# Performance work log

Hardware: AMD Instinct MI355X
Metric: run time of the kernel (lower is better)

The kernel has to match this reference:

```python
import jax, jax.numpy as jnp
import numpy as np
from jax import lax

QBITS = 8  # per layer_configs: 8-bit weights and activations


def fake_quant(x, bits=QBITS):
    """Per-tensor symmetric fake quantization with straight-through estimator."""
    qmax = float(2 ** (bits - 1) - 1)  # 127 for 8-bit
    scale = jnp.maximum(jnp.max(jnp.abs(x)), 1e-8) / qmax
    q = jnp.clip(jnp.round(x / scale), -qmax - 1.0, qmax) * scale
    # STE: forward uses q, backward passes gradient through unchanged
    return x + lax.stop_gradient(q - x)


def qconv(x, w, b):
    """Fake-quantized conv: quantize activations and weights, then VALID conv + bias."""
    xq = fake_quant(x)
    wq = fake_quant(w)
    y = lax.conv_general_dilated(
        xq, wq, window_strides=(1, 1), padding='VALID',
        dimension_numbers=('NCHW', 'OIHW', 'NCHW'))
    return y + b[None, :, None, None]


def setup_inputs() -> dict:
    key = jax.random.key(0)
    ks = jax.random.split(key, 9)
    return {
        'x':  jax.random.uniform(ks[0], (256, 1, 128, 128), dtype=jnp.float32),
        'w1': jax.random.normal(ks[1], (16, 1, 3, 3), dtype=jnp.float32) * 0.3,
        'b1': jax.random.normal(ks[2], (16,), dtype=jnp.float32) * 0.05,
        'w2': jax.random.normal(ks[3], (16, 16, 3, 3), dtype=jnp.float32) * 0.1,
        'b2': jax.random.normal(ks[4], (16,), dtype=jnp.float32) * 0.05,
        'w3': jax.random.normal(ks[5], (16, 16, 3, 3), dtype=jnp.float32) * 0.1,
        'b3': jax.random.normal(ks[6], (16,), dtype=jnp.float32) * 0.05,
        'w4': jax.random.normal(ks[7], (1, 16, 2, 2), dtype=jnp.float32) * 0.1,
        'b4': jax.random.normal(ks[8], (1,), dtype=jnp.float32) * 0.05,
    }


def reference(x, w1, b1, w2, b2, w3, b3, w4, b4):
    # x: [N,1,128,128] -> [N,16,126,126] -> [N,16,124,124] -> [N,16,122,122] -> [N,1,121,121]
    h = jax.nn.relu(qconv(x, w1, b1))
    h = jax.nn.relu(qconv(h, w2, b2))
    h = jax.nn.relu(qconv(h, w3, b3))
    return jax.nn.sigmoid(qconv(h, w4, b4))
```

## Files before the change

kernel.cpp:

```cpp
#include <hip/hip_runtime.h>
#include <math.h>
#include <limits.h>


#define THREADS 256

typedef __attribute__((ext_vector_type(4))) int i32x4;

__device__ __forceinline__ int xcd_swz(int bid, int nwg) {
    return (bid & 7) * (nwg >> 3) + (bid >> 3);
}
__device__ __forceinline__ int swzb(int rec) {
    return (rec << 4) ^ ((rec & 56) << 1);
}

__device__ __forceinline__ float block_reduce_max(float m, float* wred) {
#pragma unroll
    for (int off = 32; off > 0; off >>= 1)
        m = fmaxf(m, __shfl_down(m, off, 64));
    if ((threadIdx.x & 63) == 0) wred[threadIdx.x >> 6] = m;
    __syncthreads();
    return fmaxf(fmaxf(wred[0], wred[1]), fmaxf(wred[2], wred[3]));
}

__global__ void init_kernel(unsigned int* slots) {
    if (threadIdx.x < 8) slots[threadIdx.x] = 0u;
}

__global__ void fill_kernel(float* out, int n, float v) {
    int i = blockIdx.x * blockDim.x + threadIdx.x;
    int stride = gridDim.x * blockDim.x;
    for (; i < n; i += stride) out[i] = v;
}

__global__ __launch_bounds__(THREADS) void absmax4_kernel(
    const float4* __restrict__ x, int n4, unsigned int* __restrict__ slot) {
    __shared__ float wred[4];
    float m = 0.f;
    const int stride = gridDim.x * blockDim.x;
    for (int i = blockIdx.x * blockDim.x + threadIdx.x; i < n4; i += stride) {
        float4 v = x[i];
        m = fmaxf(fmaxf(fabsf(v.x), fabsf(v.y)),
                  fmaxf(fmaxf(fabsf(v.z), fabsf(v.w)), m));
    }
    m = block_reduce_max(m, wred);
    if (threadIdx.x == 0) atomicMax(slot, __float_as_uint(m));
}

__global__ __launch_bounds__(THREADS) void quant_w_kernel(
    const float* __restrict__ w1, const float* __restrict__ w2,
    const float* __restrict__ w3, const float* __restrict__ w4,
    int* __restrict__ qw1p, signed char* __restrict__ wi8_2,
    signed char* __restrict__ wi8_3, signed char* __restrict__ wi8_4,
    unsigned int* __restrict__ slots) {
    __shared__ float wred[4];
    const float* w; int nel;
    switch (blockIdx.x) {
        case 0:  w = w1; nel = 144;  break;
        case 1:  w = w2; nel = 2304; break;
        case 2:  w = w3; nel = 2304; break;
        default: w = w4; nel = 64;   break;
    }
    float m = 0.f;
    for (int i = threadIdx.x; i < nel; i += blockDim.x)
        m = fmaxf(m, fabsf(w[i]));
    m = block_reduce_max(m, wred);
    if (threadIdx.x == 0) slots[4 + blockIdx.x] = __float_as_uint(m);
    const float s = fmaxf(m, 1e-8f) / 127.0f;

    if (blockIdx.x == 0) {
        if (threadIdx.x < 64) {
            int qq = threadIdx.x >> 4, co = threadIdx.x & 15;
            unsigned pk = 0u;
            if (qq < 3) {
#pragma unroll
                for (int dx = 0; dx < 3; ++dx) {
                    float qv = fminf(fmaxf(rintf(w[co * 9 + qq * 3 + dx] / s),
                                           -128.f), 127.f);
                    pk |= ((unsigned)(int)qv & 0xffu) << (8 * dx);
                }
            }
            qw1p[threadIdx.x] = (int)pk;
        }
    } else if (blockIdx.x == 3) {
        for (int i = threadIdx.x; i < 1024; i += blockDim.x) {
            int ci = i & 15, lane = (i >> 4) & 63;
            int tap = lane >> 4, ky = tap >> 1, kx = tap & 1;
            float v = fminf(fmaxf(rintf(w[(ci * 2 + ky) * 2 + kx] / s),
                                  -128.f), 127.f);
            wi8_4[i] = (signed char)(int)v;
        }
    } else {
        signed char* wi8 = (blockIdx.x == 1) ? wi8_2 : wi8_3;
        for (int i = threadIdx.x; i < 3072; i += blockDim.x) {
            int ci = i & 15, lane = (i >> 4) & 63, g = i >> 10;
            int co = lane & 15, qq = lane >> 4;
            int pos = 4 * g + qq;
            float v = 0.f;
            if (pos < 9) {
                int ky = pos / 3, kx = pos % 3;
                v = fminf(fmaxf(rintf(w[((co * 16 + ci) * 3 + ky) * 3 + kx] / s),
                                -128.f), 127.f);
            }
            wi8[i] = (signed char)(int)v;
        }
    }
}

__global__ __launch_bounds__(THREADS) void c1max_kernel(
    const float* __restrict__ x, const int* __restrict__ qw1p,
    const float* __restrict__ b1, unsigned int* __restrict__ slots) {
    __shared__ signed char xq[40 * 40];
    __shared__ float wred[4];
    const int bid = xcd_swz(blockIdx.x, gridDim.x);
    const int n = bid >> 4, tr = bid & 15;
    const int ty = (tr >> 2) * 32, tx = (tr & 3) * 32;
    const int tid = threadIdx.x, lane = tid & 63, wv = tid >> 6;
    const int q = lane >> 4, col = lane & 15;

    const float s_x = fmaxf(__uint_as_float(slots[0]), 1e-8f) / 127.0f;
    const float sw1 = fmaxf(__uint_as_float(slots[4]), 1e-8f) / 127.0f;
    const float sxw1 = s_x * sw1;
    const float* xN = x + (size_t)n * 128 * 128;

    for (int i = tid; i < 1296; i += THREADS) {
        int iy = i / 36, ix = i - iy * 36;
        int gy = min(ty + iy, 127), gx = min(tx + ix, 127);
        float qf = rintf(xN[gy * 128 + gx] / s_x);
        qf = fminf(fmaxf(qf, -128.f), 127.f);
        xq[iy * 40 + ix] = (signed char)(int)qf;
    }
    i32x4 a1 = {qw1p[q * 16 + col], 0, 0, 0};
    __syncthreads();

    bool okx[3];
#pragma unroll
    for (int g3 = 0; g3 < 3; ++g3) {
        int pxx = g3 * 16 + col;
        okx[g3] = (pxx < 34) && (tx + pxx <= 125);
    }
    int mi[4] = {INT_MIN, INT_MIN, INT_MIN, INT_MIN};
    for (int py = wv; py < 34; py += 4) {
        const bool oky = (ty + py <= 125);
#pragma unroll
        for (int g3 = 0; g3 < 3; ++g3) {
            const int pxx = g3 * 16 + col;
            const int base = (py + q) * 40 + (pxx & ~3);
            unsigned lo = *(const unsigned*)(xq + base);
            unsigned hi = *(const unsigned*)(xq + base + 4);
            unsigned win = (unsigned)((((unsigned long long)hi << 32) | lo)
                                      >> ((pxx & 3) * 8));
            i32x4 b = {(int)win, 0, 0, 0};
            i32x4 z = {0, 0, 0, 0};
            i32x4 acc = __builtin_amdgcn_mfma_i32_16x16x64_i8(a1, b, z, 0, 0, 0);
            if (oky && okx[g3]) {
#pragma unroll
                for (int j = 0; j < 4; ++j)
                    mi[j] = (acc[j] > mi[j]) ? acc[j] : mi[j];
            }
        }
    }
    float m = 0.f;
#pragma unroll
    for (int j = 0; j < 4; ++j)
        m = fmaxf(m, fmaxf(fmaf((float)mi[j], sxw1, b1[q * 4 + j]), 0.f));
    m = block_reduce_max(m, wred);
    if (tid == 0) atomicMax(&slots[1], __float_as_uint(m));
}

__global__ __launch_bounds__(THREADS) void k3_kernel(
    const float* __restrict__ x, const int* __restrict__ qw1p,
    const float* __restrict__ b1, signed char* __restrict__ h1out,
    const signed char* __restrict__ wi8_2, const float* __restrict__ b2,
    unsigned int* __restrict__ slots) {
    __shared__ signed char xq[40 * 40];
    __shared__ signed char h1t[34 * 34 * 16 + 128];
    __shared__ float wred[4];
    const int bid = xcd_swz(blockIdx.x, gridDim.x);
    const int n = bid >> 4, tr = bid & 15;
    const int ty = (tr >> 2) * 32, tx = (tr & 3) * 32;
    const int tid = threadIdx.x, lane = tid & 63, wv = tid >> 6;
    const int q = lane >> 4, col = lane & 15;

    const float s_x  = fmaxf(__uint_as_float(slots[0]), 1e-8f) / 127.0f;
    const float sw1  = fmaxf(__uint_as_float(slots[4]), 1e-8f) / 127.0f;
    const float r1   = 127.0f / fmaxf(__uint_as_float(slots[1]), 1e-8f);
    const float A1   = (s_x * sw1) * r1;
    const float* xN = x + (size_t)n * 128 * 128;

    for (int i = tid; i < 1296; i += THREADS) {
        int iy = i / 36, ix = i - iy * 36;
        int gy = min(ty + iy, 127), gx = min(tx + ix, 127);
        float qf = rintf(xN[gy * 128 + gx] / s_x);
        qf = fminf(fmaxf(qf, -128.f), 127.f);
        xq[iy * 40 + ix] = (signed char)(int)qf;
    }

    i32x4 a1 = {qw1p[q * 16 + col], 0, 0, 0};
    i32x4 af2[3];
#pragma unroll
    for (int g = 0; g < 3; ++g)
        af2[g] = ((const i32x4*)wi8_2)[g * 64 + lane];
    float B1j[4], b2j[4];
#pragma unroll
    for (int j = 0; j < 4; ++j) {
        B1j[j] = b1[q * 4 + j] * r1;
        b2j[j] = b2[q * 4 + j];
    }
    __syncthreads();

    bool okx[3];
#pragma unroll
    for (int g3 = 0; g3 < 3; ++g3) {
        int pxx = g3 * 16 + col;
        okx[g3] = (pxx < 34) && (tx + pxx <= 125);
    }
    for (int py = wv; py < 34; py += 4) {
        const bool oky = (ty + py <= 125);
#pragma unroll
        for (int g3 = 0; g3 < 3; ++g3) {
            const int pxx = g3 * 16 + col;
            const int base = (py + q) * 40 + (pxx & ~3);
            unsigned lo = *(const unsigned*)(xq + base);
            unsigned hi = *(const unsigned*)(xq + base + 4);
            unsigned win = (unsigned)((((unsigned long long)hi << 32) | lo)
                                      >> ((pxx & 3) * 8));
            i32x4 b = {(int)win, 0, 0, 0};
            i32x4 z = {0, 0, 0, 0};
            i32x4 acc = __builtin_amdgcn_mfma_i32_16x16x64_i8(a1, b, z, 0, 0, 0);
            if (pxx < 34) {
                unsigned pk = 0u;
#pragma unroll
                for (int j = 0; j < 4; ++j) {
                    float t = fmaf((float)acc[j], A1, B1j[j]);
                    float q8 = fminf(fmaxf(rintf(t), 0.f), 127.f);
                    pk |= ((unsigned)(int)q8) << (j * 8);
                }
                *(unsigned*)(h1t + swzb(py * 34 + pxx) + q * 4) = pk;
                if (oky && okx[g3])
                    *(unsigned*)(h1out +
                        ((size_t)(n * 126 + ty + py) * 126 + tx + pxx) * 16
                        + q * 4) = pk;
            }
        }
    }
    __syncthreads();

    const int wr = wv >> 1, wc = wv & 1;
    int drec[3];
#pragma unroll
    for (int g = 0; g < 3; ++g) {
        int pos = 4 * g + q;
        int dy = (pos < 9) ? pos / 3 : 0;
        int dx = (pos < 9) ? pos % 3 : 0;
        drec[g] = dy * 34 + dx;
    }
    const int ix2 = 16 * wc + col;
    const bool okc = (tx + ix2 <= 123);
    const int rlim2 = 123 - ty - 16 * wr;
    int mi[4] = {INT_MIN, INT_MIN, INT_MIN, INT_MIN};

#pragma unroll 4
    for (int r = 0; r < 16; ++r) {
        const int rec = (16 * wr + r) * 34 + ix2;
        i32x4 acc = {0, 0, 0, 0};
#pragma unroll
        for (int g = 0; g < 3; ++g) {
            i32x4 b = *(const i32x4*)(h1t + swzb(rec + drec[g]));
            acc = __builtin_amdgcn_mfma_i32_16x16x64_i8(af2[g], b, acc, 0, 0, 0);
        }
        if (okc && r <= rlim2) {
#pragma unroll
            for (int j = 0; j < 4; ++j)
                mi[j] = (acc[j] > mi[j]) ? acc[j] : mi[j];
        }
    }
    const float s1  = fmaxf(__uint_as_float(slots[1]), 1e-8f) / 127.0f;
    const float sw2 = fmaxf(__uint_as_float(slots[5]), 1e-8f) / 127.0f;
    const float sxw = s1 * sw2;
    float m = 0.f;
#pragma unroll
    for (int j = 0; j < 4; ++j)
        m = fmaxf(m, fmaxf(fmaf((float)mi[j], sxw, b2j[j]), 0.f));
    m = block_reduce_max(m, wred);
    if (tid == 0) atomicMax(&slots[2], __float_as_uint(m));
}

__global__ __launch_bounds__(THREADS) void k4_kernel(
    const signed char* __restrict__ h1, const signed char* __restrict__ wi8_2,
    const float* __restrict__ b2, signed char* __restrict__ h2out,
    const signed char* __restrict__ wi8_3, const float* __restrict__ b3,
    unsigned int* __restrict__ slots) {
    __shared__ signed char h1t[34 * 34 * 16 + 128];
    __shared__ signed char h2t[32 * 32 * 16 + 128];
    __shared__ float wred[4];
    const int bid = xcd_swz(blockIdx.x, gridDim.x);
    const int n = bid / 25, tr = bid % 25;
    const int ty = (tr / 5) * 30, tx = (tr % 5) * 30;
    const int tid = threadIdx.x, lane = tid & 63, wv = tid >> 6;
    const int q = lane >> 4, col = lane & 15;
    const int wr = wv >> 1, wc = wv & 1;

    const signed char* h1N = h1 + (size_t)n * 126 * 126 * 16;
#pragma unroll
    for (int it = 0; it < 5; ++it) {
        int p = it * 256 + tid;
        if (p < 1156) {
            int iy = p / 34, ix = p - iy * 34;
            int gy = min(ty + iy, 125), gx = min(tx + ix, 125);
            *(int4*)(h1t + swzb(p)) =
                *(const int4*)(h1N + ((size_t)gy * 126 + gx) * 16);
        }
    }
    i32x4 af2[3], af3[3];
#pragma unroll
    for (int g = 0; g < 3; ++g) {
        af2[g] = ((const i32x4*)wi8_2)[g * 64 + lane];
        af3[g] = ((const i32x4*)wi8_3)[g * 64 + lane];
    }
    __syncthreads();

    int d34[3], d32[3];
#pragma unroll
    for (int g = 0; g < 3; ++g) {
        int pos = 4 * g + q;
        int dy = (pos < 9) ? pos / 3 : 0;
        int dx = (pos < 9) ? pos % 3 : 0;
        d34[g] = dy * 34 + dx;
        d32[g] = dy * 32 + dx;
    }
    const float s1  = fmaxf(__uint_as_float(slots[1]), 1e-8f) / 127.0f;
    const float sw2 = fmaxf(__uint_as_float(slots[5]), 1e-8f) / 127.0f;
    const float r2  = 127.0f / fmaxf(__uint_as_float(slots[2]), 1e-8f);
    const float A2  = (s1 * sw2) * r2;
    float B2j[4], b3j[4];
#pragma unroll
    for (int j = 0; j < 4; ++j) {
        B2j[j] = b2[q * 4 + j] * r2;
        b3j[j] = b3[q * 4 + j];
    }

    const int ix2 = 16 * wc + col;
    signed char* h2N = h2out + (size_t)n * 124 * 124 * 16;
    const bool gxok = (tx + ix2 <= 123);
    const int rlim = 123 - ty - 16 * wr;
    int goff = ((ty + 16 * wr) * 124 + tx + ix2) * 16 + q * 4;

#pragma unroll 4
    for (int r = 0; r < 16; ++r) {
        const int iy2 = 16 * wr + r;
        const int rec = iy2 * 34 + ix2;
        i32x4 acc = {0, 0, 0, 0};
#pragma unroll
        for (int g = 0; g < 3; ++g) {
            i32x4 b = *(const i32x4*)(h1t + swzb(rec + d34[g]));
            acc = __builtin_amdgcn_mfma_i32_16x16x64_i8(af2[g], b, acc, 0, 0, 0);
        }
        unsigned pk = 0u;
#pragma unroll
        for (int j = 0; j < 4; ++j) {
            float t = fmaf((float)acc[j], A2, B2j[j]);
            float q8 = fminf(fmaxf(rintf(t), 0.f), 127.f);
            pk |= ((unsigned)(int)q8) << (j * 8);
        }
        *(unsigned*)(h2t + swzb(iy2 * 32 + ix2) + q * 4) = pk;
        if (gxok && r <= rlim)
            *(unsigned*)(h2N + goff) = pk;
        goff += 124 * 16;
    }
    __syncthreads();

    const bool okc3 = (ix2 <= 29) && (tx + ix2 <= 121);
    const int rlim3 = min(29, 121 - ty) - 16 * wr;
    int mi[4] = {INT_MIN, INT_MIN, INT_MIN, INT_MIN};
#pragma unroll 4
    for (int r = 0; r < 16; ++r) {
        const int iy3 = 16 * wr + r;
        if (iy3 <= 29) {
            const int rec = iy3 * 32 + ix2;
            i32x4 acc = {0, 0, 0, 0};
#pragma unroll
            for (int g = 0; g < 3; ++g) {
                i32x4 b = *(const i32x4*)(h2t + swzb(rec + d32[g]));
                acc = __builtin_amdgcn_mfma_i32_16x16x64_i8(af3[g], b, acc, 0, 0, 0);
            }
            if (okc3 && r <= rlim3) {
#pragma unroll
                for (int j = 0; j < 4; ++j)
                    mi[j] = (acc[j] > mi[j]) ? acc[j] : mi[j];
            }
        }
    }
    const float s2  = fmaxf(__uint_as_float(slots[2]), 1e-8f) / 127.0f;
    const float sw3 = fmaxf(__uint_as_float(slots[6]), 1e-8f) / 127.0f;
    const float sxw3 = s2 * sw3;
    float m = 0.f;
#pragma unroll
    for (int j = 0; j < 4; ++j)
        m = fmaxf(m, fmaxf(fmaf((float)mi[j], sxw3, b3j[j]), 0.f));
    m = block_reduce_max(m, wred);
    if (tid == 0) atomicMax(&slots[3], __float_as_uint(m));
}

__global__ __launch_bounds__(THREADS) void k5_kernel(
    const signed char* __restrict__ h2, const signed char* __restrict__ wi8_3,
    const float* __restrict__ b3, const signed char* __restrict__ wi8_4,
    const float* __restrict__ b4, float* __restrict__ out,
    unsigned int* __restrict__ slots) {
    __shared__ signed char h2t[34 * 34 * 16 + 128];
    __shared__ signed char h3t[32 * 32 * 16 + 128];
    const int bid = xcd_swz(blockIdx.x, gridDim.x);
    const int n = bid / 25, tr = bid % 25;
    const int ty = (tr / 5) * 30, tx = (tr % 5) * 30;
    const int tid = threadIdx.x, lane = tid & 63, wv = tid >> 6;
    const int q = lane >> 4, col = lane & 15;
    const int wr = wv >> 1, wc = wv & 1;

    const signed char* h2N = h2 + (size_t)n * 124 * 124 * 16;
#pragma unroll
    for (int it = 0; it < 5; ++it) {
        int p = it * 256 + tid;
        if (p < 1156) {
            int iy = p / 34, ix = p - iy * 34;
            int gy = min(ty + iy, 123), gx = min(tx + ix, 123);
            *(int4*)(h2t + swzb(p)) =
                *(const int4*)(h2N + ((size_t)gy * 124 + gx) * 16);
        }
    }
    i32x4 af3[3];
#pragma unroll
    for (int g = 0; g < 3; ++g)
        af3[g] = ((const i32x4*)wi8_3)[g * 64 + lane];
    i32x4 a4 = ((const i32x4*)wi8_4)[lane];
    __syncthreads();

    int d34[3];
#pragma unroll
    for (int g = 0; g < 3; ++g) {
        int pos = 4 * g + q;
        int dy = (pos < 9) ? pos / 3 : 0;
        int dx = (pos < 9) ? pos % 3 : 0;
        d34[g] = dy * 34 + dx;
    }
    const float s2  = fmaxf(__uint_as_float(slots[2]), 1e-8f) / 127.0f;
    const float sw3 = fmaxf(__uint_as_float(slots[6]), 1e-8f) / 127.0f;
    const float r3  = 127.0f / fmaxf(__uint_as_float(slots[3]), 1e-8f);
    const float A3  = (s2 * sw3) * r3;
    float B3j[4];
#pragma unroll
    for (int j = 0; j < 4; ++j) B3j[j] = b3[q * 4 + j] * r3;
    const int ix3 = 16 * wc + col;

#pragma unroll 4
    for (int r = 0; r < 16; ++r) {
        const int iy3 = 16 * wr + r;
        const int rec = iy3 * 34 + ix3;
        i32x4 acc = {0, 0, 0, 0};
#pragma unroll
        for (int g = 0; g < 3; ++g) {
            i32x4 b = *(const i32x4*)(h2t + swzb(rec + d34[g]));
            acc = __builtin_amdgcn_mfma_i32_16x16x64_i8(af3[g], b, acc, 0, 0, 0);
        }
        unsigned pk = 0u;
#pragma unroll
        for (int j = 0; j < 4; ++j) {
            float t = fmaf((float)acc[j], A3, B3j[j]);
            float q8 = fminf(fmaxf(rintf(t), 0.f), 127.f);
            pk |= ((unsigned)(int)q8) << (j * 8);
        }
        *(unsigned*)(h3t + swzb(iy3 * 32 + ix3) + q * 4) = pk;
    }
    __syncthreads();

    const float s3  = fmaxf(__uint_as_float(slots[3]), 1e-8f) / 127.0f;
    const float sw4 = fmaxf(__uint_as_float(slots[7]), 1e-8f) / 127.0f;
    const float sy4 = s3 * sw4;
    const float b40 = b4[0];
    const int ky4 = q >> 1, kx4 = q & 1;
    float* outN = out + (size_t)n * 121 * 121;

    for (int r = wv; r < 31; r += 4) {
#pragma unroll
        for (int seg = 0; seg < 2; ++seg) {
            const int c = seg * 16 + col;
            const int rec = (r + ky4) * 32 + c + kx4;
            i32x4 b = *(const i32x4*)(h3t + swzb(rec));
            i32x4 z = {0, 0, 0, 0};
            i32x4 acc = __builtin_amdgcn_mfma_i32_16x16x64_i8(a4, b, z, 0, 0, 0);
            if (q == 0 && c <= 30 && ty + r <= 120 && tx + c <= 120) {
                float yv = fmaf((float)acc[0], sy4, b40);
                outN[(size_t)(ty + r) * 121 + tx + c] =
                    1.0f / (1.0f + expf(-yv));
            }
        }
    }
}

extern "C" void kernel_launch(void* const* d_in, const int* in_sizes, int n_in,
                              void* d_out, int out_size, void* d_ws, size_t ws_size,
                              hipStream_t stream) {
    (void)in_sizes; (void)n_in;
    const float* x  = (const float*)d_in[0];
    const float* w1 = (const float*)d_in[1];
    const float* b1 = (const float*)d_in[2];
    const float* w2 = (const float*)d_in[3];
    const float* b2 = (const float*)d_in[4];
    const float* w3 = (const float*)d_in[5];
    const float* b3 = (const float*)d_in[6];
    const float* w4 = (const float*)d_in[7];
    const float* b4 = (const float*)d_in[8];

    char* ws = (char*)d_ws;
    unsigned int* slots = (unsigned int*)ws;
    int* qw1p = (int*)(ws + 256);
    signed char* wi8_2 = (signed char*)(ws + 2048);
    signed char* wi8_3 = (signed char*)(ws + 5120);
    signed char* wi8_4 = (signed char*)(ws + 8192);

    const size_t Q1 = 65028096ULL;
    const size_t Q2 = 62980096ULL;
    signed char* qb1 = (signed char*)(ws + 32768);
    signed char* qb2 = (signed char*)(ws + 32768 + Q1);
    float* outp = (float*)d_out;

    const size_t need = 32768ULL + Q1 + Q2;
    if (ws_size < need) {
        float v = 100.0f + (float)(ws_size >> 20);
        hipLaunchKernelGGL(fill_kernel, dim3(1024), dim3(THREADS), 0, stream,
                           outp, out_size, v);
        return;
    }

    hipLaunchKernelGGL(init_kernel, dim3(1), dim3(64), 0, stream, slots);
    hipLaunchKernelGGL(absmax4_kernel, dim3(2048), dim3(THREADS), 0, stream,
                       (const float4*)x, 256 * 128 * 128 / 4, slots + 0);
    hipLaunchKernelGGL(quant_w_kernel, dim3(4), dim3(THREADS), 0, stream,
                       w1, w2, w3, w4, qw1p, wi8_2, wi8_3, wi8_4, slots);

    hipLaunchKernelGGL(c1max_kernel, dim3(256 * 16), dim3(THREADS), 0, stream,
                       x, qw1p, b1, slots);
    hipLaunchKernelGGL(k3_kernel, dim3(256 * 16), dim3(THREADS), 0, stream,
                       x, qw1p, b1, qb1, wi8_2, b2, slots);
    const int fgrid = 256 * 25;
    hipLaunchKernelGGL(k4_kernel, dim3(fgrid), dim3(THREADS), 0, stream,
                       qb1, wi8_2, b2, qb2, wi8_3, b3, slots);
    hipLaunchKernelGGL(k5_kernel, dim3(fgrid), dim3(THREADS), 0, stream,
                       qb2, wi8_3, b3, wi8_4, b4, outp, slots);
}
```

Baseline: 317.0 us.

## Cache quantized input tiles in workspace and use padded LDS row strides

The first conv pass now writes its int8-quantized input tile to a global scratch buffer (aliased onto the later h2 buffer), so the fused conv1+conv2 kernel copies those bytes instead of re-reading and re-quantizing the fp32 input. Separately, the XOR-swizzled LDS addressing for the 16-byte channel records is replaced with padded row strides (35 and 33 records per row) to avoid bank conflicts with simpler address arithmetic. This trades the 4-byte-per-pixel fp32 reread and division for a 1-byte write plus read, and relies on the padding removing conflicts as well as the swizzle did.

Result: no change. 317.6 us (median of 2 runs) (+0.2%).

```diff
diff --git a/kernel.cpp b/kernel.cpp
--- a/kernel.cpp
+++ b/kernel.cpp
@@ -10,9 +10,8 @@
 __device__ __forceinline__ int xcd_swz(int bid, int nwg) {
     return (bid & 7) * (nwg >> 3) + (bid >> 3);
 }
-__device__ __forceinline__ int swzb(int rec) {
-    return (rec << 4) ^ ((rec & 56) << 1);
-}
+__device__ __forceinline__ int a35(int iy, int ix) { return (iy * 35 + ix) << 4; }
+__device__ __forceinline__ int a33(int iy, int ix) { return (iy * 33 + ix) << 4; }
 
 __device__ __forceinline__ float block_reduce_max(float m, float* wred) {
 #pragma unroll
@@ -109,7 +108,8 @@
 
 __global__ __launch_bounds__(THREADS) void c1max_kernel(
     const float* __restrict__ x, const int* __restrict__ qw1p,
-    const float* __restrict__ b1, unsigned int* __restrict__ slots) {
+    const float* __restrict__ b1, signed char* __restrict__ xq8g,
+    unsigned int* __restrict__ slots) {
     __shared__ signed char xq[40 * 40];
     __shared__ float wred[4];
     const int bid = xcd_swz(blockIdx.x, gridDim.x);
@@ -122,13 +122,16 @@
     const float sw1 = fmaxf(__uint_as_float(slots[4]), 1e-8f) / 127.0f;
     const float sxw1 = s_x * sw1;
     const float* xN = x + (size_t)n * 128 * 128;
+    signed char* xq8b = xq8g + (size_t)bid * 1600;
 
     for (int i = tid; i < 1296; i += THREADS) {
         int iy = i / 36, ix = i - iy * 36;
         int gy = min(ty + iy, 127), gx = min(tx + ix, 127);
         float qf = rintf(xN[gy * 128 + gx] / s_x);
         qf = fminf(fmaxf(qf, -128.f), 127.f);
-        xq[iy * 40 + ix] = (signed char)(int)qf;
+        signed char b = (signed char)(int)qf;
+        xq[iy * 40 + ix] = b;
+        xq8b[iy * 40 + ix] = b;
     }
     i32x4 a1 = {qw1p[q * 16 + col], 0, 0, 0};
     __syncthreads();
@@ -169,12 +172,12 @@
 }
 
 __global__ __launch_bounds__(THREADS) void k3_kernel(
-    const float* __restrict__ x, const int* __restrict__ qw1p,
+    const signed char* __restrict__ xq8g, const int* __restrict__ qw1p,
     const float* __restrict__ b1, signed char* __restrict__ h1out,
     const signed char* __restrict__ wi8_2, const float* __restrict__ b2,
     unsigned int* __restrict__ slots) {
     __shared__ signed char xq[40 * 40];
-    __shared__ signed char h1t[34 * 34 * 16 + 128];
+    __shared__ signed char h1t[34 * 35 * 16];
     __shared__ float wred[4];
     const int bid = xcd_swz(blockIdx.x, gridDim.x);
     const int n = bid >> 4, tr = bid & 15;
@@ -186,15 +189,10 @@
     const float sw1  = fmaxf(__uint_as_float(slots[4]), 1e-8f) / 127.0f;
     const float r1   = 127.0f / fmaxf(__uint_as_float(slots[1]), 1e-8f);
     const float A1   = (s_x * sw1) * r1;
-    const float* xN = x + (size_t)n * 128 * 128;
-
-    for (int i = tid; i < 1296; i += THREADS) {
-        int iy = i / 36, ix = i - iy * 36;
-        int gy = min(ty + iy, 127), gx = min(tx + ix, 127);
-        float qf = rintf(xN[gy * 128 + gx] / s_x);
-        qf = fminf(fmaxf(qf, -128.f), 127.f);
-        xq[iy * 40 + ix] = (signed char)(int)qf;
-    }
+
+    const signed char* xq8b = xq8g + (size_t)bid * 1600;
+    for (int j = tid; j < 100; j += THREADS)
+        *(int4*)(xq + j * 16) = *(const int4*)(xq8b + j * 16);
 
     i32x4 a1 = {qw1p[q * 16 + col], 0, 0, 0};
     i32x4 af2[3];
@@ -236,7 +234,7 @@
                     float q8 = fminf(fmaxf(rintf(t), 0.f), 127.f);
                     pk |= ((unsigned)(int)q8) << (j * 8);
                 }
-                *(unsigned*)(h1t + swzb(py * 34 + pxx) + q * 4) = pk;
+                *(unsigned*)(h1t + a35(py, pxx) + q * 4) = pk;
                 if (oky && okx[g3])
                     *(unsigned*)(h1out +
                         ((size_t)(n * 126 + ty + py) * 126 + tx + pxx) * 16
@@ -247,13 +245,12 @@
     __syncthreads();
 
     const int wr = wv >> 1, wc = wv & 1;
-    int drec[3];
+    int dyg[3], dxg[3];
 #pragma unroll
     for (int g = 0; g < 3; ++g) {
         int pos = 4 * g + q;
-        int dy = (pos < 9) ? pos / 3 : 0;
-        int dx = (pos < 9) ? pos % 3 : 0;
-        drec[g] = dy * 34 + dx;
+        dyg[g] = (pos < 9) ? pos / 3 : 0;
+        dxg[g] = (pos < 9) ? pos % 3 : 0;
     }
     const int ix2 = 16 * wc + col;
     const bool okc = (tx + ix2 <= 123);
@@ -262,11 +259,11 @@
 
 #pragma unroll 4
     for (int r = 0; r < 16; ++r) {
-        const int rec = (16 * wr + r) * 34 + ix2;
+        const int iy2 = 16 * wr + r;
         i32x4 acc = {0, 0, 0, 0};
 #pragma unroll
         for (int g = 0; g < 3; ++g) {
-            i32x4 b = *(const i32x4*)(h1t + swzb(rec + drec[g]));
+            i32x4 b = *(const i32x4*)(h1t + a35(iy2 + dyg[g], ix2 + dxg[g]));
             acc = __builtin_amdgcn_mfma_i32_16x16x64_i8(af2[g], b, acc, 0, 0, 0);
         }
         if (okc && r <= rlim2) {
@@ -291,8 +288,8 @@
     const float* __restrict__ b2, signed char* __restrict__ h2out,
     const signed char* __restrict__ wi8_3, const float* __restrict__ b3,
     unsigned int* __restrict__ slots) {
-    __shared__ signed char h1t[34 * 34 * 16 + 128];
-    __shared__ signed char h2t[32 * 32 * 16 + 128];
+    __shared__ signed char h1t[34 * 35 * 16];
+    __shared__ signed char h2t[32 * 33 * 16];
     __shared__ float wred[4];
     const int bid = xcd_swz(blockIdx.x, gridDim.x);
     const int n = bid / 25, tr = bid % 25;
@@ -308,7 +305,7 @@
         if (p < 1156) {
             int iy = p / 34, ix = p - iy * 34;
             int gy = min(ty + iy, 125), gx = min(tx + ix, 125);
-            *(int4*)(h1t + swzb(p)) =
+            *(int4*)(h1t + a35(iy, ix)) =
                 *(const int4*)(h1N + ((size_t)gy * 126 + gx) * 16);
         }
     }
@@ -320,14 +317,12 @@
     }
     __syncthreads();
 
-    int d34[3], d32[3];
+    int dyg[3], dxg[3];
 #pragma unroll
     for (int g = 0; g < 3; ++g) {
         int pos = 4 * g + q;
-        int dy = (pos < 9) ? pos / 3 : 0;
-        int dx = (pos < 9) ? pos % 3 : 0;
-        d34[g] = dy * 34 + dx;
-        d32[g] = dy * 32 + dx;
+        dyg[g] = (pos < 9) ? pos / 3 : 0;
+        dxg[g] = (pos < 9) ? pos % 3 : 0;
     }
     const float s1  = fmaxf(__uint_as_float(slots[1]), 1e-8f) / 127.0f;
     const float sw2 = fmaxf(__uint_as_float(slots[5]), 1e-8f) / 127.0f;
@@ -349,11 +344,10 @@
 #pragma unroll 4
     for (int r = 0; r < 16; ++r) {
         const int iy2 = 16 * wr + r;
-        const int rec = iy2 * 34 + ix2;
         i32x4 acc = {0, 0, 0, 0};
 #pragma unroll
         for (int g = 0; g < 3; ++g) {
-            i32x4 b = *(const i32x4*)(h1t + swzb(rec + d34[g]));
+            i32x4 b = *(const i32x4*)(h1t + a35(iy2 + dyg[g], ix2 + dxg[g]));
             acc = __builtin_amdgcn_mfma_i32_16x16x64_i8(af2[g], b, acc, 0, 0, 0);
         }
         unsigned pk = 0u;
@@ -363,7 +357,7 @@
             float q8 = fminf(fmaxf(rintf(t), 0.f), 127.f);
             pk |= ((unsigned)(int)q8) << (j * 8);
         }
-        *(unsigned*)(h2t + swzb(iy2 * 32 + ix2) + q * 4) = pk;
+        *(unsigned*)(h2t + a33(iy2, ix2) + q * 4) = pk;
         if (gxok && r <= rlim)
             *(unsigned*)(h2N + goff) = pk;
         goff += 124 * 16;
@@ -377,11 +371,10 @@
     for (int r = 0; r < 16; ++r) {
         const int iy3 = 16 * wr + r;
         if (iy3 <= 29) {
-            const int rec = iy3 * 32 + ix2;
             i32x4 acc = {0, 0, 0, 0};
 #pragma unroll
             for (int g = 0; g < 3; ++g) {
-                i32x4 b = *(const i32x4*)(h2t + swzb(rec + d32[g]));
+                i32x4 b = *(const i32x4*)(h2t + a33(iy3 + dyg[g], ix2 + dxg[g]));
                 acc = __builtin_amdgcn_mfma_i32_16x16x64_i8(af3[g], b, acc, 0, 0, 0);
             }
             if (okc3 && r <= rlim3) {
@@ -407,8 +400,8 @@
     const float* __restrict__ b3, const signed char* __restrict__ wi8_4,
     const float* __restrict__ b4, float* __restrict__ out,
     unsigned int* __restrict__ slots) {
-    __shared__ signed char h2t[34 * 34 * 16 + 128];
-    __shared__ signed char h3t[32 * 32 * 16 + 128];
+    __shared__ signed char h2t[34 * 35 * 16];
+    __shared__ signed char h3t[32 * 33 * 16];
     const int bid = xcd_swz(blockIdx.x, gridDim.x);
     const int n = bid / 25, tr = bid % 25;
     const int ty = (tr / 5) * 30, tx = (tr % 5) * 30;
@@ -423,7 +416,7 @@
         if (p < 1156) {
             int iy = p / 34, ix = p - iy * 34;
             int gy = min(ty + iy, 123), gx = min(tx + ix, 123);
-            *(int4*)(h2t + swzb(p)) =
+            *(int4*)(h2t + a35(iy, ix)) =
                 *(const int4*)(h2N + ((size_t)gy * 124 + gx) * 16);
         }
     }
@@ -434,13 +427,12 @@
     i32x4 a4 = ((const i32x4*)wi8_4)[lane];
     __syncthreads();
 
-    int d34[3];
+    int dyg[3], dxg[3];
 #pragma unroll
     for (int g = 0; g < 3; ++g) {
         int pos = 4 * g + q;
-        int dy = (pos < 9) ? pos / 3 : 0;
-        int dx = (pos < 9) ? pos % 3 : 0;
-        d34[g] = dy * 34 + dx;
+        dyg[g] = (pos < 9) ? pos / 3 : 0;
+        dxg[g] = (pos < 9) ? pos % 3 : 0;
     }
     const float s2  = fmaxf(__uint_as_float(slots[2]), 1e-8f) / 127.0f;
     const float sw3 = fmaxf(__uint_as_float(slots[6]), 1e-8f) / 127.0f;
@@ -454,11 +446,10 @@
 #pragma unroll 4
     for (int r = 0; r < 16; ++r) {
         const int iy3 = 16 * wr + r;
-        const int rec = iy3 * 34 + ix3;
         i32x4 acc = {0, 0, 0, 0};
 #pragma unroll
         for (int g = 0; g < 3; ++g) {
-            i32x4 b = *(const i32x4*)(h2t + swzb(rec + d34[g]));
+            i32x4 b = *(const i32x4*)(h2t + a35(iy3 + dyg[g], ix3 + dxg[g]));
             acc = __builtin_amdgcn_mfma_i32_16x16x64_i8(af3[g], b, acc, 0, 0, 0);
         }
         unsigned pk = 0u;
@@ -468,7 +459,7 @@
             float q8 = fminf(fmaxf(rintf(t), 0.f), 127.f);
             pk |= ((unsigned)(int)q8) << (j * 8);
         }
-        *(unsigned*)(h3t + swzb(iy3 * 32 + ix3) + q * 4) = pk;
+        *(unsigned*)(h3t + a33(iy3, ix3) + q * 4) = pk;
     }
     __syncthreads();
 
@@ -483,8 +474,7 @@
 #pragma unroll
         for (int seg = 0; seg < 2; ++seg) {
             const int c = seg * 16 + col;
-            const int rec = (r + ky4) * 32 + c + kx4;
-            i32x4 b = *(const i32x4*)(h3t + swzb(rec));
+            i32x4 b = *(const i32x4*)(h3t + a33(r + ky4, c + kx4));
             i32x4 z = {0, 0, 0, 0};
             i32x4 acc = __builtin_amdgcn_mfma_i32_16x16x64_i8(a4, b, z, 0, 0, 0);
             if (q == 0 && c <= 30 && ty + r <= 120 && tx + c <= 120) {
@@ -521,6 +511,7 @@
     const size_t Q2 = 62980096ULL;
     signed char* qb1 = (signed char*)(ws + 32768);
     signed char* qb2 = (signed char*)(ws + 32768 + Q1);
+    signed char* xq8 = qb2;
     float* outp = (float*)d_out;
 
     const size_t need = 32768ULL + Q1 + Q2;
@@ -538,9 +529,9 @@
                        w1, w2, w3, w4, qw1p, wi8_2, wi8_3, wi8_4, slots);
 
     hipLaunchKernelGGL(c1max_kernel, dim3(256 * 16), dim3(THREADS), 0, stream,
-                       x, qw1p, b1, slots);
+                       x, qw1p, b1, xq8, slots);
     hipLaunchKernelGGL(k3_kernel, dim3(256 * 16), dim3(THREADS), 0, stream,
-                       x, qw1p, b1, qb1, wi8_2, b2, slots);
+                       xq8, qw1p, b1, qb1, wi8_2, b2, slots);
     const int fgrid = 256 * 25;
     hipLaunchKernelGGL(k4_kernel, dim3(fgrid), dim3(THREADS), 0, stream,
                        qb1, wi8_2, b2, qb2, wi8_3, b3, slots);
```
